# Kernel tuning notes

Measured on AMD Instinct MI355X. Metric: run time of the kernel, lower is better.

## Reference

```python
import jax, jax.numpy as jnp
import numpy as np

N = 20000          # num nodes
DEG = 8            # directed avg degree before symmetrization
IN_C, HID, OUT_C, K = 128, 32, 16, 2


def _build_graph(n, deg, seed=0):
    """Build symmetric 1-hop A1 (no self loops) and exact 2-hop A2 edge lists,
    with D^{-1/2} A D^{-1/2} normalized values (mirrors _prepare_prop)."""
    rng = np.random.default_rng(seed)
    e = n * deg
    row = rng.integers(0, n, e)
    col = rng.integers(0, n, e)
    r = np.concatenate([row, col])
    c = np.concatenate([col, row])
    m = r != c
    keys1 = np.unique(r[m].astype(np.int64) * n + c[m])  # A1 = indicator(A - I)
    r1 = (keys1 // n).astype(np.int64)
    c1 = (keys1 % n).astype(np.int64)
    # exact 2-hop: nonzeros of A1@A1, minus A1 and diagonal
    degs = np.bincount(r1, minlength=n)
    indptr = np.concatenate([np.zeros(1, np.int64), np.cumsum(degs)])
    counts = degs[c1]                       # per edge (u,v): deg(v)
    cum = np.cumsum(counts)
    total = int(cum[-1])
    offs = np.arange(total) - np.repeat(cum - counts, counts)
    dst2 = c1[np.repeat(indptr[c1], counts) + offs]
    src2 = np.repeat(r1, counts)
    keys2 = np.unique(src2 * n + dst2)
    diag = np.arange(n, dtype=np.int64) * (n + 1)
    keys2 = np.setdiff1d(keys2, np.concatenate([keys1, diag]), assume_unique=True)
    r2 = (keys2 // n).astype(np.int64)
    c2 = (keys2 % n).astype(np.int64)

    def norm(rr, cc):  # D^{-1/2} A D^{-1/2} on binary symmetric adjacency
        d = np.bincount(rr, minlength=n).astype(np.float64)
        dis = np.where(d > 0, 1.0 / np.sqrt(np.maximum(d, 1.0)), 0.0)
        return (dis[rr] * dis[cc]).astype(np.float32)

    return r1, c1, norm(r1, c1), r2, c2, norm(r2, c2)


def setup_inputs() -> dict:
    key = jax.random.key(0)
    k1, k2, k3 = jax.random.split(key, 3)
    x = jax.random.normal(k1, (N, IN_C), dtype=jnp.float32)
    # xavier_uniform for the two dense weights
    ae = float(np.sqrt(6.0 / (IN_C + HID)))
    cdim = (2 ** (K + 1) - 1) * HID  # 224
    ac = float(np.sqrt(6.0 / (cdim + OUT_C)))
    w_embed = jax.random.uniform(k2, (IN_C, HID), jnp.float32, -ae, ae)
    w_classify = jax.random.uniform(k3, (cdim, OUT_C), jnp.float32, -ac, ac)
    r1, c1, v1, r2, c2, v2 = _build_graph(N, DEG)
    return {
        "x": x, "w_embed": w_embed, "w_classify": w_classify,
        "a1_row": jnp.asarray(r1), "a1_col": jnp.asarray(c1), "a1_val": jnp.asarray(v1),
        "a2_row": jnp.asarray(r2), "a2_col": jnp.asarray(c2), "a2_val": jnp.asarray(v2),
    }


def _spmm(row, col, val, x, n):
    # sparse @ dense: gather source rows, scale, scatter-add into dest rows
    return jax.ops.segment_sum(x[col] * val[:, None], row, num_segments=n)


def reference(x, w_embed, w_classify, a1_row, a1_col, a1_val, a2_row, a2_col, a2_val):
    n = x.shape[0]
    rs = [jax.nn.relu(x @ w_embed)]  # [N, HID]
    for _ in range(K):
        r = rs[-1]
        r1 = _spmm(a1_row, a1_col, a1_val, r, n)
        r2 = _spmm(a2_row, a2_col, a2_val, r, n)
        rs.append(jax.nn.relu(jnp.concatenate([r1, r2], axis=1)))
    r_final = jnp.concatenate(rs, axis=1)  # [N, 7*HID]; dropout is identity in eval
    return r_final @ w_classify            # [N, OUT_C]
```

## Files before the change

### kernel.cpp

```cpp
#include <hip/hip_runtime.h>

typedef unsigned int uint;
typedef unsigned short ushort;

#define IN_C 128
#define HID  32

__device__ __forceinline__ float bf_lo(uint u) { return __uint_as_float(u << 16); }
__device__ __forceinline__ float bf_hi(uint u) { return __uint_as_float(u & 0xffff0000u); }
__device__ __forceinline__ uint  f2bf(float f) {
    uint u = __float_as_uint(f);
    return (u + 0x7fffu + ((u >> 16) & 1u)) >> 16;
}
__device__ __forceinline__ float inv_sqrt_deg(int d) {
    return d > 0 ? 1.f / sqrtf((float)d) : 0.f;
}

__global__ void prep_kernel(const float* __restrict__ x,
                            const float* __restrict__ w,
                            ushort* __restrict__ r0,
                            const int* __restrict__ a1r, int E1, int* __restrict__ ip1,
                            const int* __restrict__ a2r, int E2, int* __restrict__ ip2,
                            const int* __restrict__ a2c, const float* __restrict__ a2v,
                            float* __restrict__ dummy,
                            int n, int nbE, int nbI, int nbT) {
    __shared__ float wl[IN_C * HID];
    const int tid = threadIdx.x;
    if (blockIdx.x < nbE) {
        for (int i = tid; i < IN_C * HID; i += blockDim.x) wl[i] = w[i];
        __syncthreads();
        const int row = blockIdx.x * 16 + tid / 16;
        const int h0  = (tid % 16) * 2;
        if (row >= n) return;
        const float4* xr = (const float4*)(x + (size_t)row * IN_C);
        float a0 = 0.f, a1 = 0.f;
#pragma unroll
        for (int k4 = 0; k4 < IN_C / 4; ++k4) {
            float4 xv = xr[k4];
            a0 += xv.x * wl[(4*k4+0)*HID + h0];  a1 += xv.x * wl[(4*k4+0)*HID + h0+1];
            a0 += xv.y * wl[(4*k4+1)*HID + h0];  a1 += xv.y * wl[(4*k4+1)*HID + h0+1];
            a0 += xv.z * wl[(4*k4+2)*HID + h0];  a1 += xv.z * wl[(4*k4+2)*HID + h0+1];
            a0 += xv.w * wl[(4*k4+3)*HID + h0];  a1 += xv.w * wl[(4*k4+3)*HID + h0+1];
        }
        uint p = f2bf(fmaxf(a0, 0.f)) | (f2bf(fmaxf(a1, 0.f)) << 16);
        ((uint*)r0)[(size_t)row * 16 + (tid % 16)] = p;
    } else if (blockIdx.x < nbE + nbI) {
        const int i = (blockIdx.x - nbE) * 256 + tid;
        if (i > n) return;
        int lo = 0, hi = E1;
        while (lo < hi) { int m = (lo + hi) >> 1; if (a1r[m] < i) lo = m + 1; else hi = m; }
        ip1[i] = lo;
        lo = 0; hi = E2;
        while (lo < hi) { int m = (lo + hi) >> 1; if (a2r[m] < i) lo = m + 1; else hi = m; }
        ip2[i] = lo;
    } else {
        const int t = (blockIdx.x - nbE - nbI) * 256 + tid;
        const int stride = nbT * 256;
        const int total4 = E2 / 4;
        const float4* c4 = (const float4*)a2c;
        const float4* v4 = (const float4*)a2v;
        float s = 0.f;
        for (int i = t; i < total4; i += stride) {
            float4 u = c4[i], v = v4[i];
            s += u.x + u.y + u.z + u.w + v.x + v.y + v.z + v.w;
        }
        if (s == 123.456f) dummy[0] = s;
    }
}

template <int C, int ROWS, bool WITHVAL, bool SCALED>
__global__ __launch_bounds__(256) void spmm_level(
        const int* __restrict__ ip1, const int* __restrict__ col1,
        const float* __restrict__ val1,
        const int* __restrict__ ip2, const int* __restrict__ col2,
        const float* __restrict__ val2,
        const ushort* __restrict__ xin1, const ushort* __restrict__ xin2,
        ushort* __restrict__ rout,
        ushort* __restrict__ yout1, ushort* __restrict__ yout2,
        int n, int nb2) {
    constexpr int L    = C / 8;
    constexpr int SUBL = 64 / ROWS;
    constexpr int W    = SUBL / L;
    const int lane = threadIdx.x & 63;
    const int wave = threadIdx.x >> 6;
    const int sub  = lane / SUBL;
    const int li   = lane % SUBL;
    const int fl   = li % L;
    const int way  = li / L;

    int bid = blockIdx.x;
    const int* ip; const int* col; const float* val; const ushort* yin; int off;
    if (bid < nb2) {             ip = ip2; col = col2; val = val2; yin = xin2; off = C; }
    else           { bid -= nb2; ip = ip1; col = col1; val = val1; yin = xin1; off = 0; }

    const int row = (bid * 4 + wave) * ROWS + sub;
    if (row >= n) return;

    const ushort* xbase = yin + fl * 8;
    float acc[8];
#pragma unroll
    for (int j = 0; j < 8; ++j) acc[j] = 0.f;

    auto gat = [&](int c) -> uint4 {
        return *(const uint4*)(xbase + (size_t)c * C);
    };
    auto fmadd = [&](const uint4& u, float v) {
        acc[0] += v * bf_lo(u.x); acc[1] += v * bf_hi(u.x);
        acc[2] += v * bf_lo(u.y); acc[3] += v * bf_hi(u.y);
        acc[4] += v * bf_lo(u.z); acc[5] += v * bf_hi(u.z);
        acc[6] += v * bf_lo(u.w); acc[7] += v * bf_hi(u.w);
    };
    auto aadd = [&](const uint4& u) {
        acc[0] += bf_lo(u.x); acc[1] += bf_hi(u.x);
        acc[2] += bf_lo(u.y); acc[3] += bf_hi(u.y);
        acc[4] += bf_lo(u.z); acc[5] += bf_hi(u.z);
        acc[6] += bf_lo(u.w); acc[7] += bf_hi(u.w);
    };

    const int s = ip[row];
    const int e = ip[row + 1];
    int sv = (s + 3) & ~3; if (sv > e) sv = e;
    const int nv = (e - sv) / (4 * W);

    for (int idx = s + way; idx < sv; idx += W) {
        if (WITHVAL) fmadd(gat(col[idx]), val[idx]); else aadd(gat(col[idx]));
    }
    const int*   cb = col + sv;
    const float* vb = val + sv;
    for (int i = 0; i < nv; ++i) {
        const int base = (i * W + way) * 4;
        const int4 cc = *(const int4*)(cb + base);
        if (WITHVAL) {
            const float4 vv = *(const float4*)(vb + base);
            const uint4 g0 = gat(cc.x), g1 = gat(cc.y), g2 = gat(cc.z), g3 = gat(cc.w);
            fmadd(g0, vv.x); fmadd(g1, vv.y); fmadd(g2, vv.z); fmadd(g3, vv.w);
        } else {
            const uint4 g0 = gat(cc.x), g1 = gat(cc.y), g2 = gat(cc.z), g3 = gat(cc.w);
            aadd(g0); aadd(g1); aadd(g2); aadd(g3);
        }
    }
    for (int idx = sv + nv * 4 * W + way; idx < e; idx += W) {
        if (WITHVAL) fmadd(gat(col[idx]), val[idx]); else aadd(gat(col[idx]));
    }

#pragma unroll
    for (int m = L; m < SUBL; m <<= 1)
#pragma unroll
        for (int j = 0; j < 8; ++j) acc[j] += __shfl_xor(acc[j], m, 64);

    if (way == 0) {
        float r[8];
        if (WITHVAL) {
#pragma unroll
            for (int j = 0; j < 8; ++j) r[j] = fmaxf(acc[j], 0.f);
        } else {
            const float dsown = inv_sqrt_deg(e - s);
#pragma unroll
            for (int j = 0; j < 8; ++j) r[j] = fmaxf(dsown * acc[j], 0.f);
        }

        const size_t oidx = (size_t)row * (2 * C) + off + fl * 8;
        uint4 p;
        p.x = f2bf(r[0]) | (f2bf(r[1]) << 16);
        p.y = f2bf(r[2]) | (f2bf(r[3]) << 16);
        p.z = f2bf(r[4]) | (f2bf(r[5]) << 16);
        p.w = f2bf(r[6]) | (f2bf(r[7]) << 16);
        *(uint4*)(rout + oidx) = p;

        if (SCALED) {
            const float s1 = inv_sqrt_deg(ip1[row + 1] - ip1[row]);
            const float s2 = inv_sqrt_deg(ip2[row + 1] - ip2[row]);
            uint4 q1, q2;
            q1.x = f2bf(s1*r[0]) | (f2bf(s1*r[1]) << 16);
            q1.y = f2bf(s1*r[2]) | (f2bf(s1*r[3]) << 16);
            q1.z = f2bf(s1*r[4]) | (f2bf(s1*r[5]) << 16);
            q1.w = f2bf(s1*r[6]) | (f2bf(s1*r[7]) << 16);
            q2.x = f2bf(s2*r[0]) | (f2bf(s2*r[1]) << 16);
            q2.y = f2bf(s2*r[2]) | (f2bf(s2*r[3]) << 16);
            q2.z = f2bf(s2*r[4]) | (f2bf(s2*r[5]) << 16);
            q2.w = f2bf(s2*r[6]) | (f2bf(s2*r[7]) << 16);
            *(uint4*)(yout1 + oidx) = q1;
            *(uint4*)(yout2 + oidx) = q2;
        }
    }
}

#define CDIM 224
#define OUT_C 16
__global__ void classify_kernel(const ushort* __restrict__ r0,
                                const ushort* __restrict__ r1,
                                const ushort* __restrict__ r2,
                                const float* __restrict__ w,
                                float* __restrict__ out, int n) {
    __shared__ float wl[CDIM * OUT_C];
    const int tid = threadIdx.x;
    for (int i = tid; i < CDIM * OUT_C; i += blockDim.x) wl[i] = w[i];
    __syncthreads();
    const int row = blockIdx.x * 16 + tid / 16;
    const int o   = tid % 16;
    if (row >= n) return;
    float acc = 0.f;

    const uint4* a = (const uint4*)(r0 + (size_t)row * 32);
#pragma unroll
    for (int q = 0; q < 4; ++q) {
        uint4 u = a[q]; int j = q * 8;
        acc += bf_lo(u.x) * wl[(j+0)*OUT_C + o];  acc += bf_hi(u.x) * wl[(j+1)*OUT_C + o];
        acc += bf_lo(u.y) * wl[(j+2)*OUT_C + o];  acc += bf_hi(u.y) * wl[(j+3)*OUT_C + o];
        acc += bf_lo(u.z) * wl[(j+4)*OUT_C + o];  acc += bf_hi(u.z) * wl[(j+5)*OUT_C + o];
        acc += bf_lo(u.w) * wl[(j+6)*OUT_C + o];  acc += bf_hi(u.w) * wl[(j+7)*OUT_C + o];
    }
    const uint4* b = (const uint4*)(r1 + (size_t)row * 64);
#pragma unroll
    for (int q = 0; q < 8; ++q) {
        uint4 u = b[q]; int j = 32 + q * 8;
        acc += bf_lo(u.x) * wl[(j+0)*OUT_C + o];  acc += bf_hi(u.x) * wl[(j+1)*OUT_C + o];
        acc += bf_lo(u.y) * wl[(j+2)*OUT_C + o];  acc += bf_hi(u.y) * wl[(j+3)*OUT_C + o];
        acc += bf_lo(u.z) * wl[(j+4)*OUT_C + o];  acc += bf_hi(u.z) * wl[(j+5)*OUT_C + o];
        acc += bf_lo(u.w) * wl[(j+6)*OUT_C + o];  acc += bf_hi(u.w) * wl[(j+7)*OUT_C + o];
    }
    const uint4* c = (const uint4*)(r2 + (size_t)row * 128);
#pragma unroll
    for (int q = 0; q < 16; ++q) {
        uint4 u = c[q]; int j = 96 + q * 8;
        acc += bf_lo(u.x) * wl[(j+0)*OUT_C + o];  acc += bf_hi(u.x) * wl[(j+1)*OUT_C + o];
        acc += bf_lo(u.y) * wl[(j+2)*OUT_C + o];  acc += bf_hi(u.y) * wl[(j+3)*OUT_C + o];
        acc += bf_lo(u.z) * wl[(j+4)*OUT_C + o];  acc += bf_hi(u.z) * wl[(j+5)*OUT_C + o];
        acc += bf_lo(u.w) * wl[(j+6)*OUT_C + o];  acc += bf_hi(u.w) * wl[(j+7)*OUT_C + o];
    }
    out[(size_t)row * OUT_C + o] = acc;
}

extern "C" void kernel_launch(void* const* d_in, const int* in_sizes, int n_in,
                              void* d_out, int out_size, void* d_ws, size_t ws_size,
                              hipStream_t stream) {
    const float* x   = (const float*)d_in[0];
    const float* we  = (const float*)d_in[1];
    const float* wc  = (const float*)d_in[2];
    const int*   a1r = (const int*)  d_in[3];
    const int*   a1c = (const int*)  d_in[4];
    const float* a1v = (const float*)d_in[5];
    const int*   a2r = (const int*)  d_in[6];
    const int*   a2c = (const int*)  d_in[7];
    const float* a2v = (const float*)d_in[8];
    float* out = (float*)d_out;

    const int E1 = in_sizes[3];
    const int E2 = in_sizes[6];
    const int n  = in_sizes[0] / IN_C;

    ushort* r0   = (ushort*)d_ws;
    ushort* r1   = r0   + (size_t)n * 32;
    ushort* r2   = r1   + (size_t)n * 64;
    ushort* y1_1 = r2   + (size_t)n * 128;
    ushort* y2_1 = y1_1 + (size_t)n * 64;
    int*    ip1  = (int*)(y2_1 + (size_t)n * 64);
    int*    ip2  = ip1 + (n + 1);
    float*  dummy = (float*)(ip2 + (n + 1));

    {
        const int nbE = (n + 15) / 16;
        const int nbI = (n + 1 + 255) / 256;
        const int nbT = 512;
        prep_kernel<<<nbE + nbI + nbT, 256, 0, stream>>>(
            x, we, r0, a1r, E1, ip1, a2r, E2, ip2, a2c, a2v, dummy,
            n, nbE, nbI, nbT);
    }
    {
        const int nb = (n + 7) / 8;
        spmm_level<32, 2, true, true><<<2 * nb, 256, 0, stream>>>(
            ip1, a1c, a1v, ip2, a2c, a2v, r0, r0, r1, y1_1, y2_1, n, nb);
    }
    {
        const int nb = (n + 3) / 4;
        spmm_level<64, 1, false, false><<<2 * nb, 256, 0, stream>>>(
            ip1, a1c, nullptr, ip2, a2c, nullptr, y1_1, y2_1, r2,
            nullptr, nullptr, n, nb);
    }
    classify_kernel<<<(n + 15) / 16, 256, 0, stream>>>(r0, r1, r2, wc, out, n);
}
```

Baseline: 221.0 us.

## Fuse second-hop SpMM with final classifier and drop r2 intermediate buffer

```diff
diff --git a/kernel.cpp b/kernel.cpp
--- a/kernel.cpp
+++ b/kernel.cpp
@@ -5,6 +5,8 @@
 
 #define IN_C 128
 #define HID  32
+#define CDIM 224
+#define OUT_C 16
 
 __device__ __forceinline__ float bf_lo(uint u) { return __uint_as_float(u << 16); }
 __device__ __forceinline__ float bf_hi(uint u) { return __uint_as_float(u & 0xffff0000u); }
@@ -68,13 +70,13 @@
     }
 }
 
-template <int C, int ROWS, bool WITHVAL, bool SCALED>
-__global__ __launch_bounds__(256) void spmm_level(
+template <int C, int ROWS>
+__global__ __launch_bounds__(256) void spmm_l1(
         const int* __restrict__ ip1, const int* __restrict__ col1,
         const float* __restrict__ val1,
         const int* __restrict__ ip2, const int* __restrict__ col2,
         const float* __restrict__ val2,
-        const ushort* __restrict__ xin1, const ushort* __restrict__ xin2,
+        const ushort* __restrict__ xin,
         ushort* __restrict__ rout,
         ushort* __restrict__ yout1, ushort* __restrict__ yout2,
         int n, int nb2) {
@@ -89,59 +91,43 @@
     const int way  = li / L;
 
     int bid = blockIdx.x;
-    const int* ip; const int* col; const float* val; const ushort* yin; int off;
-    if (bid < nb2) {             ip = ip2; col = col2; val = val2; yin = xin2; off = C; }
-    else           { bid -= nb2; ip = ip1; col = col1; val = val1; yin = xin1; off = 0; }
+    const int* ip; const int* col; const float* val; int off;
+    if (bid < nb2) {             ip = ip2; col = col2; val = val2; off = C; }
+    else           { bid -= nb2; ip = ip1; col = col1; val = val1; off = 0; }
 
     const int row = (bid * 4 + wave) * ROWS + sub;
     if (row >= n) return;
 
-    const ushort* xbase = yin + fl * 8;
+    const ushort* xbase = xin + fl * 8;
     float acc[8];
 #pragma unroll
     for (int j = 0; j < 8; ++j) acc[j] = 0.f;
 
-    auto gat = [&](int c) -> uint4 {
-        return *(const uint4*)(xbase + (size_t)c * C);
-    };
+    auto gat = [&](int c) -> uint4 { return *(const uint4*)(xbase + (size_t)c * C); };
     auto fmadd = [&](const uint4& u, float v) {
         acc[0] += v * bf_lo(u.x); acc[1] += v * bf_hi(u.x);
         acc[2] += v * bf_lo(u.y); acc[3] += v * bf_hi(u.y);
         acc[4] += v * bf_lo(u.z); acc[5] += v * bf_hi(u.z);
         acc[6] += v * bf_lo(u.w); acc[7] += v * bf_hi(u.w);
     };
-    auto aadd = [&](const uint4& u) {
-        acc[0] += bf_lo(u.x); acc[1] += bf_hi(u.x);
-        acc[2] += bf_lo(u.y); acc[3] += bf_hi(u.y);
-        acc[4] += bf_lo(u.z); acc[5] += bf_hi(u.z);
-        acc[6] += bf_lo(u.w); acc[7] += bf_hi(u.w);
-    };
 
     const int s = ip[row];
     const int e = ip[row + 1];
     int sv = (s + 3) & ~3; if (sv > e) sv = e;
     const int nv = (e - sv) / (4 * W);
 
-    for (int idx = s + way; idx < sv; idx += W) {
-        if (WITHVAL) fmadd(gat(col[idx]), val[idx]); else aadd(gat(col[idx]));
-    }
+    for (int idx = s + way; idx < sv; idx += W) fmadd(gat(col[idx]), val[idx]);
     const int*   cb = col + sv;
     const float* vb = val + sv;
     for (int i = 0; i < nv; ++i) {
         const int base = (i * W + way) * 4;
-        const int4 cc = *(const int4*)(cb + base);
-        if (WITHVAL) {
-            const float4 vv = *(const float4*)(vb + base);
-            const uint4 g0 = gat(cc.x), g1 = gat(cc.y), g2 = gat(cc.z), g3 = gat(cc.w);
-            fmadd(g0, vv.x); fmadd(g1, vv.y); fmadd(g2, vv.z); fmadd(g3, vv.w);
-        } else {
-            const uint4 g0 = gat(cc.x), g1 = gat(cc.y), g2 = gat(cc.z), g3 = gat(cc.w);
-            aadd(g0); aadd(g1); aadd(g2); aadd(g3);
-        }
-    }
-    for (int idx = sv + nv * 4 * W + way; idx < e; idx += W) {
-        if (WITHVAL) fmadd(gat(col[idx]), val[idx]); else aadd(gat(col[idx]));
-    }
+        const int4   cc = *(const int4*)  (cb + base);
+        const float4 vv = *(const float4*)(vb + base);
+        const uint4 g0 = gat(cc.x), g1 = gat(cc.y), g2 = gat(cc.z), g3 = gat(cc.w);
+        fmadd(g0, vv.x); fmadd(g1, vv.y); fmadd(g2, vv.z); fmadd(g3, vv.w);
+    }
+    for (int idx = sv + nv * 4 * W + way; idx < e; idx += W)
+        fmadd(gat(col[idx]), val[idx]);
 
 #pragma unroll
     for (int m = L; m < SUBL; m <<= 1)
@@ -150,14 +136,8 @@
 
     if (way == 0) {
         float r[8];
-        if (WITHVAL) {
-#pragma unroll
-            for (int j = 0; j < 8; ++j) r[j] = fmaxf(acc[j], 0.f);
-        } else {
-            const float dsown = inv_sqrt_deg(e - s);
-#pragma unroll
-            for (int j = 0; j < 8; ++j) r[j] = fmaxf(dsown * acc[j], 0.f);
-        }
+#pragma unroll
+        for (int j = 0; j < 8; ++j) r[j] = fmaxf(acc[j], 0.f);
 
         const size_t oidx = (size_t)row * (2 * C) + off + fl * 8;
         uint4 p;
@@ -167,68 +147,135 @@
         p.w = f2bf(r[6]) | (f2bf(r[7]) << 16);
         *(uint4*)(rout + oidx) = p;
 
-        if (SCALED) {
-            const float s1 = inv_sqrt_deg(ip1[row + 1] - ip1[row]);
-            const float s2 = inv_sqrt_deg(ip2[row + 1] - ip2[row]);
-            uint4 q1, q2;
-            q1.x = f2bf(s1*r[0]) | (f2bf(s1*r[1]) << 16);
-            q1.y = f2bf(s1*r[2]) | (f2bf(s1*r[3]) << 16);
-            q1.z = f2bf(s1*r[4]) | (f2bf(s1*r[5]) << 16);
-            q1.w = f2bf(s1*r[6]) | (f2bf(s1*r[7]) << 16);
-            q2.x = f2bf(s2*r[0]) | (f2bf(s2*r[1]) << 16);
-            q2.y = f2bf(s2*r[2]) | (f2bf(s2*r[3]) << 16);
-            q2.z = f2bf(s2*r[4]) | (f2bf(s2*r[5]) << 16);
-            q2.w = f2bf(s2*r[6]) | (f2bf(s2*r[7]) << 16);
-            *(uint4*)(yout1 + oidx) = q1;
-            *(uint4*)(yout2 + oidx) = q2;
+        const float s1 = inv_sqrt_deg(ip1[row + 1] - ip1[row]);
+        const float s2 = inv_sqrt_deg(ip2[row + 1] - ip2[row]);
+        uint4 q1, q2;
+        q1.x = f2bf(s1*r[0]) | (f2bf(s1*r[1]) << 16);
+        q1.y = f2bf(s1*r[2]) | (f2bf(s1*r[3]) << 16);
+        q1.z = f2bf(s1*r[4]) | (f2bf(s1*r[5]) << 16);
+        q1.w = f2bf(s1*r[6]) | (f2bf(s1*r[7]) << 16);
+        q2.x = f2bf(s2*r[0]) | (f2bf(s2*r[1]) << 16);
+        q2.y = f2bf(s2*r[2]) | (f2bf(s2*r[3]) << 16);
+        q2.z = f2bf(s2*r[4]) | (f2bf(s2*r[5]) << 16);
+        q2.w = f2bf(s2*r[6]) | (f2bf(s2*r[7]) << 16);
+        *(uint4*)(yout1 + oidx) = q1;
+        *(uint4*)(yout2 + oidx) = q2;
+    }
+}
+
+__global__ __launch_bounds__(256) void spmm2_cls(
+        const int* __restrict__ ip1, const int* __restrict__ col1,
+        const int* __restrict__ ip2, const int* __restrict__ col2,
+        const ushort* __restrict__ y1, const ushort* __restrict__ y2,
+        const ushort* __restrict__ r0, const ushort* __restrict__ r1,
+        const float* __restrict__ w, float* __restrict__ out, int n) {
+    __shared__ float wl[CDIM * OUT_C];
+    for (int i = threadIdx.x; i < CDIM * OUT_C; i += 256) wl[i] = w[i];
+
+    const int lane = threadIdx.x & 63;
+    const int wave = threadIdx.x >> 6;
+    const int row  = blockIdx.x * 4 + wave;
+    const int fl   = lane & 7;
+    const int way  = lane >> 3;
+
+    float acc1[8], acc2[8];
+#pragma unroll
+    for (int j = 0; j < 8; ++j) { acc1[j] = 0.f; acc2[j] = 0.f; }
+    int deg1 = 0, deg2 = 0;
+
+    if (row < n) {
+        auto half = [&](const int* __restrict__ ip, const int* __restrict__ col,
+                        const ushort* __restrict__ yb, float* acc, int& deg) {
+            const int s = ip[row];
+            const int e = ip[row + 1];
+            deg = e - s;
+            const ushort* xbase = yb + fl * 8;
+            auto gat = [&](int c) -> uint4 {
+                return *(const uint4*)(xbase + (size_t)c * 64);
+            };
+            auto aadd = [&](const uint4& u) {
+                acc[0] += bf_lo(u.x); acc[1] += bf_hi(u.x);
+                acc[2] += bf_lo(u.y); acc[3] += bf_hi(u.y);
+                acc[4] += bf_lo(u.z); acc[5] += bf_hi(u.z);
+                acc[6] += bf_lo(u.w); acc[7] += bf_hi(u.w);
+            };
+            int sv = (s + 3) & ~3; if (sv > e) sv = e;
+            const int nv = (e - sv) / 32;
+            for (int idx = s + way; idx < sv; idx += 8) aadd(gat(col[idx]));
+            const int* cb = col + sv;
+            for (int i = 0; i < nv; ++i) {
+                const int base = (i * 8 + way) * 4;
+                const int4 cc = *(const int4*)(cb + base);
+                const uint4 g0 = gat(cc.x), g1 = gat(cc.y),
+                            g2 = gat(cc.z), g3 = gat(cc.w);
+                aadd(g0); aadd(g1); aadd(g2); aadd(g3);
+            }
+            for (int idx = sv + nv * 32 + way; idx < e; idx += 8) aadd(gat(col[idx]));
+        };
+        half(ip2, col2, y2, acc2, deg2);
+        half(ip1, col1, y1, acc1, deg1);
+
+#pragma unroll
+        for (int m = 8; m < 64; m <<= 1)
+#pragma unroll
+            for (int j = 0; j < 8; ++j) {
+                acc1[j] += __shfl_xor(acc1[j], m, 64);
+                acc2[j] += __shfl_xor(acc2[j], m, 64);
+            }
+    }
+
+    __syncthreads();
+    if (row >= n) return;
+
+    const float s1 = inv_sqrt_deg(deg1);
+    const float s2 = inv_sqrt_deg(deg2);
+    float r2a[8], r2b[8];
+#pragma unroll
+    for (int j = 0; j < 8; ++j) {
+        r2a[j] = fmaxf(s1 * acc1[j], 0.f);
+        r2b[j] = fmaxf(s2 * acc2[j], 0.f);
+    }
+
+    const int o0 = way * 2;
+    float q0 = 0.f, q1 = 0.f;
+#pragma unroll
+    for (int j = 0; j < 8; ++j) {
+        const int fA = (96 + fl * 8 + j) * OUT_C;
+        const int fB = (160 + fl * 8 + j) * OUT_C;
+        q0 += r2a[j] * wl[fA + o0];     q1 += r2a[j] * wl[fA + o0 + 1];
+        q0 += r2b[j] * wl[fB + o0];     q1 += r2b[j] * wl[fB + o0 + 1];
+    }
+    {
+        const uint4 u = ((const uint4*)(r1 + (size_t)row * 64))[fl];
+        float f[8];
+        f[0]=bf_lo(u.x); f[1]=bf_hi(u.x); f[2]=bf_lo(u.y); f[3]=bf_hi(u.y);
+        f[4]=bf_lo(u.z); f[5]=bf_hi(u.z); f[6]=bf_lo(u.w); f[7]=bf_hi(u.w);
+#pragma unroll
+        for (int j = 0; j < 8; ++j) {
+            const int fi = (32 + fl * 8 + j) * OUT_C;
+            q0 += f[j] * wl[fi + o0];   q1 += f[j] * wl[fi + o0 + 1];
         }
     }
-}
-
-#define CDIM 224
-#define OUT_C 16
-__global__ void classify_kernel(const ushort* __restrict__ r0,
-                                const ushort* __restrict__ r1,
-                                const ushort* __restrict__ r2,
-                                const float* __restrict__ w,
-                                float* __restrict__ out, int n) {
-    __shared__ float wl[CDIM * OUT_C];
-    const int tid = threadIdx.x;
-    for (int i = tid; i < CDIM * OUT_C; i += blockDim.x) wl[i] = w[i];
-    __syncthreads();
-    const int row = blockIdx.x * 16 + tid / 16;
-    const int o   = tid % 16;
-    if (row >= n) return;
-    float acc = 0.f;
-
-    const uint4* a = (const uint4*)(r0 + (size_t)row * 32);
-#pragma unroll
-    for (int q = 0; q < 4; ++q) {
-        uint4 u = a[q]; int j = q * 8;
-        acc += bf_lo(u.x) * wl[(j+0)*OUT_C + o];  acc += bf_hi(u.x) * wl[(j+1)*OUT_C + o];
-        acc += bf_lo(u.y) * wl[(j+2)*OUT_C + o];  acc += bf_hi(u.y) * wl[(j+3)*OUT_C + o];
-        acc += bf_lo(u.z) * wl[(j+4)*OUT_C + o];  acc += bf_hi(u.z) * wl[(j+5)*OUT_C + o];
-        acc += bf_lo(u.w) * wl[(j+6)*OUT_C + o];  acc += bf_hi(u.w) * wl[(j+7)*OUT_C + o];
-    }
-    const uint4* b = (const uint4*)(r1 + (size_t)row * 64);
-#pragma unroll
-    for (int q = 0; q < 8; ++q) {
-        uint4 u = b[q]; int j = 32 + q * 8;
-        acc += bf_lo(u.x) * wl[(j+0)*OUT_C + o];  acc += bf_hi(u.x) * wl[(j+1)*OUT_C + o];
-        acc += bf_lo(u.y) * wl[(j+2)*OUT_C + o];  acc += bf_hi(u.y) * wl[(j+3)*OUT_C + o];
-        acc += bf_lo(u.z) * wl[(j+4)*OUT_C + o];  acc += bf_hi(u.z) * wl[(j+5)*OUT_C + o];
-        acc += bf_lo(u.w) * wl[(j+6)*OUT_C + o];  acc += bf_hi(u.w) * wl[(j+7)*OUT_C + o];
-    }
-    const uint4* c = (const uint4*)(r2 + (size_t)row * 128);
-#pragma unroll
-    for (int q = 0; q < 16; ++q) {
-        uint4 u = c[q]; int j = 96 + q * 8;
-        acc += bf_lo(u.x) * wl[(j+0)*OUT_C + o];  acc += bf_hi(u.x) * wl[(j+1)*OUT_C + o];
-        acc += bf_lo(u.y) * wl[(j+2)*OUT_C + o];  acc += bf_hi(u.y) * wl[(j+3)*OUT_C + o];
-        acc += bf_lo(u.z) * wl[(j+4)*OUT_C + o];  acc += bf_hi(u.z) * wl[(j+5)*OUT_C + o];
-        acc += bf_lo(u.w) * wl[(j+6)*OUT_C + o];  acc += bf_hi(u.w) * wl[(j+7)*OUT_C + o];
-    }
-    out[(size_t)row * OUT_C + o] = acc;
+    if (fl < 4) {
+        const uint4 u = ((const uint4*)(r0 + (size_t)row * 32))[fl];
+        float f[8];
+        f[0]=bf_lo(u.x); f[1]=bf_hi(u.x); f[2]=bf_lo(u.y); f[3]=bf_hi(u.y);
+        f[4]=bf_lo(u.z); f[5]=bf_hi(u.z); f[6]=bf_lo(u.w); f[7]=bf_hi(u.w);
+#pragma unroll
+        for (int j = 0; j < 8; ++j) {
+            const int fi = (fl * 8 + j) * OUT_C;
+            q0 += f[j] * wl[fi + o0];   q1 += f[j] * wl[fi + o0 + 1];
+        }
+    }
+#pragma unroll
+    for (int m = 1; m < 8; m <<= 1) {
+        q0 += __shfl_xor(q0, m, 64);
+        q1 += __shfl_xor(q1, m, 64);
+    }
+    if (fl == 0) {
+        float2 v; v.x = q0; v.y = q1;
+        *(float2*)(out + (size_t)row * OUT_C + o0) = v;
+    }
 }
 
 extern "C" void kernel_launch(void* const* d_in, const int* in_sizes, int n_in,
@@ -251,8 +298,7 @@
 
     ushort* r0   = (ushort*)d_ws;
     ushort* r1   = r0   + (size_t)n * 32;
-    ushort* r2   = r1   + (size_t)n * 64;
-    ushort* y1_1 = r2   + (size_t)n * 128;
+    ushort* y1_1 = r1   + (size_t)n * 64;
     ushort* y2_1 = y1_1 + (size_t)n * 64;
     int*    ip1  = (int*)(y2_1 + (size_t)n * 64);
     int*    ip2  = ip1 + (n + 1);
@@ -268,14 +314,12 @@
     }
     {
         const int nb = (n + 7) / 8;
-        spmm_level<32, 2, true, true><<<2 * nb, 256, 0, stream>>>(
-            ip1, a1c, a1v, ip2, a2c, a2v, r0, r0, r1, y1_1, y2_1, n, nb);
+        spmm_l1<32, 2><<<2 * nb, 256, 0, stream>>>(
+            ip1, a1c, a1v, ip2, a2c, a2v, r0, r1, y1_1, y2_1, n, nb);
     }
     {
         const int nb = (n + 3) / 4;
-        spmm_level<64, 1, false, false><<<2 * nb, 256, 0, stream>>>(
-            ip1, a1c, nullptr, ip2, a2c, nullptr, y1_1, y2_1, r2,
-            nullptr, nullptr, n, nb);
-    }
-    classify_kernel<<<(n + 15) / 16, 256, 0, stream>>>(r0, r1, r2, wc, out, n);
-}
+        spmm2_cls<<<nb, 256, 0, stream>>>(
+            ip1, a1c, ip2, a2c, y1_1, y2_1, r0, r1, wc, out, n);
+    }
+}
```

Result: slower. 248.1 us (+12.3%).
